# Kernel optimization log

Hardware: AMD Instinct MI355X
Metric: run time of the kernel (lower is better)

The kernel has to match this reference:

```python
import jax, jax.numpy as jnp
import numpy as np

GAMMA = 2.0
CONTEXT_WINDOW = 100


def setup_inputs() -> dict:
    key = jax.random.key(0)
    k1, k2 = jax.random.split(key)
    B, S, C = 64, 131072, 3
    inputs = jax.random.normal(k1, (B, S, C), dtype=jnp.float32)
    targets = jax.random.randint(k2, (B, S), 0, C, dtype=jnp.int32)
    alpha = jnp.array([0.25, 1.0, 1.0], dtype=jnp.float32)
    return {"inputs": inputs, "targets": targets, "alpha": alpha}


def _window_mask(targets, window):
    # mask[b, i] = True iff any positive target within +/- window of i;
    # rows with no positives are fully True (matches torch loop semantics).
    B, S = targets.shape
    pos = targets > 0                                   # (B, S) bool
    cs = jnp.cumsum(pos.astype(jnp.int32), axis=1)      # inclusive prefix sums
    c = jnp.concatenate([jnp.zeros((B, 1), jnp.int32), cs], axis=1)  # (B, S+1)
    idx = jnp.arange(S)
    hi = jnp.minimum(idx + window + 1, S)               # exclusive end
    lo = jnp.maximum(idx - window, 0)                   # inclusive start
    count = c[:, hi] - c[:, lo]                         # positives in window
    mask = count > 0
    has_pos = pos.any(axis=1, keepdims=True)
    return jnp.where(has_pos, mask, True)


def reference(inputs, targets, alpha):
    # inputs: (B, S, C) logits; targets: (B, S) class indices
    mask = _window_mask(targets, CONTEXT_WINDOW)                     # (B, S)
    logp = jax.nn.log_softmax(inputs, axis=-1)                       # (B, S, C)
    ce = -jnp.take_along_axis(logp, targets[..., None].astype(jnp.int32), axis=-1)[..., 0]
    p_t = jnp.exp(-ce)
    focal = alpha[targets] * (1.0 - p_t) ** GAMMA * ce               # (B, S)
    m = mask.astype(inputs.dtype)
    # masked mean == mean over selected elements in the torch version
    return jnp.sum(focal * m) / jnp.sum(m)
```

## Files before the change

kernel.cpp:

```cpp
#include <hip/hip_runtime.h>

#define BB 64
#define SS 131072
#define WIN 100
#define TILE 4096
#define NTHREADS 256
#define TILES_PER_ROW (SS / TILE)
#define NBLOCKS (BB * TILES_PER_ROW)
#define EXT (TILE + 2*WIN)
#define NWORDS ((EXT + 63) / 64)
#define SH_BYTES (NWORDS * 64)
#define K4TOT (SH_BYTES / 4)
#define SROUNDS ((K4TOT + NTHREADS - 1) / NTHREADS)
#define NGROUPS 4

typedef float  fx4 __attribute__((ext_vector_type(4)));
typedef int    ix4 __attribute__((ext_vector_type(4)));

__device__ __forceinline__ void process4(
    const fx4 c0, const fx4 c1, const fx4 c2,
    const int j0, const unsigned long long mw, const unsigned int tpack,
    const float a0, const float a1, const float a2,
    float& fsum_m, float& fsum_a, int& cnt_m)
{
    const float xs[12] = {c0.x, c0.y, c0.z, c0.w, c1.x, c1.y, c1.z, c1.w,
                          c2.x, c2.y, c2.z, c2.w};
    #pragma unroll
    for (int j = 0; j < 4; ++j) {
        const float x0 = xs[3*j], x1 = xs[3*j+1], x2 = xs[3*j+2];
        const int tv = (tpack >> (8 * j)) & 0xFF;
        const float mx = fmaxf(x0, fmaxf(x1, x2));
        const float mn = fminf(x0, fminf(x1, x2));
        const float md = fmaxf(fminf(x0, x1), fminf(fmaxf(x0, x1), x2));
        const float emd = __expf(md - mx);
        const float emn = __expf(mn - mx);
        const float sum = 1.0f + emd + emn;
        const float xt  = (tv == 0) ? x0 : ((tv == 1) ? x1 : x2);
        const float et  = (xt == mx) ? 1.0f : ((xt == md) ? emd : emn);
        const float ce  = __logf(sum) + (mx - xt);
        const float pt  = et * __frcp_rn(sum);
        const float w   = (tv == 0) ? a0 : ((tv == 1) ? a1 : a2);
        const float om  = 1.0f - pt;
        const float focal = w * om * om * ce;
        const bool  m   = (mw >> ((j0 & 63) + j)) & 1ULL;

        fsum_a += focal;
        fsum_m += m ? focal : 0.0f;
        cnt_m  += m ? 1 : 0;
    }
}

__global__ __launch_bounds__(NTHREADS, 5) void focal_main(
    const float* __restrict__ inputs, const int* __restrict__ targets,
    const float* __restrict__ alpha, double* __restrict__ slots)
{
    __shared__ __align__(16) unsigned char sh_t[SH_BYTES];
    __shared__ unsigned long long wbits[NWORDS];
    __shared__ unsigned long long mbits[NWORDS];
    __shared__ double red[(NTHREADS/64) * 4];

    const int t = threadIdx.x;
    const int b = blockIdx.x / TILES_PER_ROW;
    const int tile = blockIdx.x % TILES_PER_ROW;
    const int s0 = tile * TILE;
    const int ext_lo = (s0 - WIN > 0) ? (s0 - WIN) : 0;
    const int ext_hi = (s0 + TILE + WIN < SS) ? (s0 + TILE + WIN) : SS;
    const int ext_len = ext_hi - ext_lo;
    const int tr_lo = s0 - ext_lo;

    const float* inrow = inputs + (long)b * SS * 3;
    const fx4* gbase = (const fx4*)(inrow + (long)s0 * 3);
    const fx4* p0 = gbase + t * 3;
    const fx4* p1 = gbase + 768 + t * 3;
    const fx4* p2 = gbase + 1536 + t * 3;
    const fx4* p3 = gbase + 2304 + t * 3;
    const fx4 q0  = __builtin_nontemporal_load(p0 + 0);
    const fx4 q1  = __builtin_nontemporal_load(p0 + 1);
    const fx4 q2  = __builtin_nontemporal_load(p0 + 2);
    const fx4 q3  = __builtin_nontemporal_load(p1 + 0);
    const fx4 q4  = __builtin_nontemporal_load(p1 + 1);
    const fx4 q5  = __builtin_nontemporal_load(p1 + 2);
    const fx4 q6  = __builtin_nontemporal_load(p2 + 0);
    const fx4 q7  = __builtin_nontemporal_load(p2 + 1);
    const fx4 q8  = __builtin_nontemporal_load(p2 + 2);
    const fx4 q9  = __builtin_nontemporal_load(p3 + 0);
    const fx4 q10 = __builtin_nontemporal_load(p3 + 1);
    const fx4 q11 = __builtin_nontemporal_load(p3 + 2);

    const float a0 = alpha[0], a1 = alpha[1], a2 = alpha[2];

    const int* trow = targets + (long)b * SS;
    #pragma unroll
    for (int it = 0; it < SROUNDS; ++it) {
        const int k4 = it * NTHREADS + t;
        if (k4 < K4TOT) {
            unsigned int pk = 0;
            if (4 * k4 < ext_len) {
                const ix4 tv4 =
                    __builtin_nontemporal_load((const ix4*)(trow + ext_lo + 4 * k4));
                pk = (unsigned)(tv4.x & 3) | ((unsigned)(tv4.y & 3) << 8) |
                     ((unsigned)(tv4.z & 3) << 16) | ((unsigned)(tv4.w & 3) << 24);
            }
            ((unsigned int*)sh_t)[k4] = pk;
        }
    }
    __syncthreads();

    int cnt_p = 0;
    if (t < NWORDS) {
        const uint4* qp = (const uint4*)(sh_t + (t << 6));
        unsigned long long wv = 0;
        #pragma unroll
        for (int r = 0; r < 4; ++r) {
            const uint4 u = qp[r];
            unsigned int x, nz;
            x = u.x; nz = (x | (x >> 1)) & 0x01010101u;
            wv |= (unsigned long long)((nz * 0x01020408u) >> 24) << (r*16 + 0);
            x = u.y; nz = (x | (x >> 1)) & 0x01010101u;
            wv |= (unsigned long long)((nz * 0x01020408u) >> 24) << (r*16 + 4);
            x = u.z; nz = (x | (x >> 1)) & 0x01010101u;
            wv |= (unsigned long long)((nz * 0x01020408u) >> 24) << (r*16 + 8);
            x = u.w; nz = (x | (x >> 1)) & 0x01010101u;
            wv |= (unsigned long long)((nz * 0x01020408u) >> 24) << (r*16 + 12);
        }
        wbits[t] = wv;
        int lo_bit = tr_lo - (t << 6);        if (lo_bit < 0) lo_bit = 0;
        int hi_bit = tr_lo + TILE - (t << 6); if (hi_bit > 64) hi_bit = 64;
        if (hi_bit > lo_bit) {
            unsigned long long rm = (hi_bit >= 64) ? ~0ULL : ((1ULL << hi_bit) - 1);
            rm &= (~0ULL << lo_bit);
            cnt_p = __popcll(wv & rm);
        }
    }
    __syncthreads();

    if (t < NWORDS) {
        const unsigned long long a = (t >= 2) ? wbits[t-2] : 0ULL;
        const unsigned long long bw = (t >= 1) ? wbits[t-1] : 0ULL;
        const unsigned long long c = wbits[t];
        const unsigned long long d = (t+1 < NWORDS) ? wbits[t+1] : 0ULL;
        const unsigned long long e = (t+2 < NWORDS) ? wbits[t+2] : 0ULL;
        unsigned long long m = c ? ~0ULL : 0ULL;
        if (d) { const int lo = __builtin_ctzll(d) - 36;
                 m |= (lo <= 0) ? ~0ULL : (~0ULL << lo); }
        if (e) { const int lo = __builtin_ctzll(e) + 28;
                 if (lo <= 63) m |= (~0ULL << lo); }
        if (bw) { const int hi = 63 - __builtin_clzll(bw) + 36;
                  m |= (hi >= 63) ? ~0ULL : (~0ULL >> (63 - hi)); }
        if (a) { const int hi = 63 - __builtin_clzll(a) - 28;
                 if (hi >= 0) m |= (hi >= 63) ? ~0ULL : (~0ULL >> (63 - hi)); }
        mbits[t] = m;
    }
    __syncthreads();

    float fsum_m = 0.0f, fsum_a = 0.0f;
    int cnt_m = 0;
    {
        int j0 = tr_lo + t * 4;
        process4(q0, q1, q2, j0, mbits[j0 >> 6],
                 *(const unsigned int*)(sh_t + j0),
                 a0, a1, a2, fsum_m, fsum_a, cnt_m);
        j0 += 1024;
        process4(q3, q4, q5, j0, mbits[j0 >> 6],
                 *(const unsigned int*)(sh_t + j0),
                 a0, a1, a2, fsum_m, fsum_a, cnt_m);
        j0 += 1024;
        process4(q6, q7, q8, j0, mbits[j0 >> 6],
                 *(const unsigned int*)(sh_t + j0),
                 a0, a1, a2, fsum_m, fsum_a, cnt_m);
        j0 += 1024;
        process4(q9, q10, q11, j0, mbits[j0 >> 6],
                 *(const unsigned int*)(sh_t + j0),
                 a0, a1, a2, fsum_m, fsum_a, cnt_m);
    }

    const int wave = t >> 6, lane = t & 63;
    #pragma unroll
    for (int off = 32; off >= 1; off >>= 1) {
        fsum_m += __shfl_down(fsum_m, off);
        fsum_a += __shfl_down(fsum_a, off);
        cnt_m  += __shfl_down(cnt_m, off);
        cnt_p  += __shfl_down(cnt_p, off);
    }
    if (lane == 0) {
        red[wave*4]   = (double)fsum_m; red[wave*4+1] = (double)cnt_m;
        red[wave*4+2] = (double)fsum_a; red[wave*4+3] = (double)cnt_p;
    }
    __syncthreads();
    if (t == 0) {
        double sm = 0, sc = 0, sa = 0, sp = 0;
        #pragma unroll
        for (int w = 0; w < NTHREADS/64; ++w) {
            sm += red[w*4]; sc += red[w*4+1]; sa += red[w*4+2]; sp += red[w*4+3];
        }
        double* slot = slots + (long)blockIdx.x * 4;
        slot[0] = sm;
        slot[1] = sc;
        slot[2] = sa;
        slot[3] = sp;
    }
}

__global__ __launch_bounds__(1024) void focal_final(
    const double* __restrict__ slots, float* __restrict__ out)
{
    __shared__ double redA[16 * 2];
    __shared__ double crs[BB];
    __shared__ double crc[BB];
    const int t = threadIdx.x;
    const int wave = t >> 6, lane = t & 63;

    double sm = 0.0, sc = 0.0;
    for (int k = t; k < NBLOCKS; k += 1024) {
        sm += slots[(long)k * 4 + 0];
        sc += slots[(long)k * 4 + 1];
    }
    #pragma unroll
    for (int off = 32; off >= 1; off >>= 1) {
        sm += __shfl_down(sm, off);
        sc += __shfl_down(sc, off);
    }
    if (lane == 0) { redA[wave*2] = sm; redA[wave*2+1] = sc; }

    const int row = t >> 4;
    const int rpart = t & 15;
    const long base = (long)row * TILES_PER_ROW + rpart * 2;
    double rs = slots[base*4 + 2] + slots[(base+1)*4 + 2];
    double rp = slots[base*4 + 3] + slots[(base+1)*4 + 3];
    #pragma unroll
    for (int off = 8; off >= 1; off >>= 1) {
        rs += __shfl_down(rs, off, 16);
        rp += __shfl_down(rp, off, 16);
    }
    if (rpart == 0) { crs[row] = rs; crc[row] = rp; }
    __syncthreads();

    if (t == 0) {
        double a = 0.0, bsum = 0.0;
        #pragma unroll
        for (int w = 0; w < 16; ++w) { a += redA[w*2]; bsum += redA[w*2+1]; }
        double corr_s = 0.0, corr_c = 0.0;
        #pragma unroll
        for (int r = 0; r < BB; ++r) {
            if (crc[r] == 0.0) { corr_s += crs[r]; corr_c += (double)SS; }
        }
        out[0] = (float)((a + corr_s) / (bsum + corr_c));
    }
}

extern "C" void kernel_launch(void* const* d_in, const int* in_sizes, int n_in,
                              void* d_out, int out_size, void* d_ws, size_t ws_size,
                              hipStream_t stream) {
    const float* inputs  = (const float*)d_in[0];
    const int*   targets = (const int*)d_in[1];
    const float* alpha   = (const float*)d_in[2];
    float* out = (float*)d_out;

    double* slots = (double*)d_ws;

    focal_main<<<NBLOCKS, NTHREADS, 0, stream>>>(inputs, targets, alpha, slots);
    focal_final<<<1, 1024, 0, stream>>>(slots, out);
}
```

Measured before the change: 178.1 us.

## Coalesce logit loads per wave and transpose through double-buffered LDS

Each wave now owns a contiguous 1024-element slice and loads it as fully coalesced fx4 chunks: lane l reads consecutive vectors instead of strided triples. The chunks are staged in a per-wave double-buffered LDS area and re-read as each lane's three vectors. Only the next group's three vectors are prefetched, not all twelve up front, which lowers register pressure but reduces loads in flight. The extra LDS round trip and reduced early memory-level parallelism may offset the better coalescing.

Measured after the change: 172.0 us. -3.4%, faster.

```diff
diff --git a/kernel.cpp b/kernel.cpp
--- a/kernel.cpp
+++ b/kernel.cpp
@@ -5,6 +5,7 @@
 #define WIN 100
 #define TILE 4096
 #define NTHREADS 256
+#define NWAVES (NTHREADS / 64)
 #define TILES_PER_ROW (SS / TILE)
 #define NBLOCKS (BB * TILES_PER_ROW)
 #define EXT (TILE + 2*WIN)
@@ -12,7 +13,8 @@
 #define SH_BYTES (NWORDS * 64)
 #define K4TOT (SH_BYTES / 4)
 #define SROUNDS ((K4TOT + NTHREADS - 1) / NTHREADS)
-#define NGROUPS 4
+#define WGROUPS 4
+#define GF4 192
 
 typedef float  fx4 __attribute__((ext_vector_type(4)));
 typedef int    ix4 __attribute__((ext_vector_type(4)));
@@ -57,9 +59,11 @@
     __shared__ __align__(16) unsigned char sh_t[SH_BYTES];
     __shared__ unsigned long long wbits[NWORDS];
     __shared__ unsigned long long mbits[NWORDS];
-    __shared__ double red[(NTHREADS/64) * 4];
+    __shared__ fx4 lbuf[NWAVES][2][GF4];
+    __shared__ double red[NWAVES * 4];
 
     const int t = threadIdx.x;
+    const int w = t >> 6, l = t & 63;
     const int b = blockIdx.x / TILES_PER_ROW;
     const int tile = blockIdx.x % TILES_PER_ROW;
     const int s0 = tile * TILE;
@@ -69,25 +73,10 @@
     const int tr_lo = s0 - ext_lo;
 
     const float* inrow = inputs + (long)b * SS * 3;
-    const fx4* gbase = (const fx4*)(inrow + (long)s0 * 3);
-    const fx4* p0 = gbase + t * 3;
-    const fx4* p1 = gbase + 768 + t * 3;
-    const fx4* p2 = gbase + 1536 + t * 3;
-    const fx4* p3 = gbase + 2304 + t * 3;
-    const fx4 q0  = __builtin_nontemporal_load(p0 + 0);
-    const fx4 q1  = __builtin_nontemporal_load(p0 + 1);
-    const fx4 q2  = __builtin_nontemporal_load(p0 + 2);
-    const fx4 q3  = __builtin_nontemporal_load(p1 + 0);
-    const fx4 q4  = __builtin_nontemporal_load(p1 + 1);
-    const fx4 q5  = __builtin_nontemporal_load(p1 + 2);
-    const fx4 q6  = __builtin_nontemporal_load(p2 + 0);
-    const fx4 q7  = __builtin_nontemporal_load(p2 + 1);
-    const fx4 q8  = __builtin_nontemporal_load(p2 + 2);
-    const fx4 q9  = __builtin_nontemporal_load(p3 + 0);
-    const fx4 q10 = __builtin_nontemporal_load(p3 + 1);
-    const fx4 q11 = __builtin_nontemporal_load(p3 + 2);
-
-    const float a0 = alpha[0], a1 = alpha[1], a2 = alpha[2];
+    const fx4* gsrc = (const fx4*)(inrow + (long)(s0 + w * 1024) * 3);
+    fx4 q0 = __builtin_nontemporal_load(gsrc + l);
+    fx4 q1 = __builtin_nontemporal_load(gsrc + 64 + l);
+    fx4 q2 = __builtin_nontemporal_load(gsrc + 128 + l);
 
     const int* trow = targets + (long)b * SS;
     #pragma unroll
@@ -153,28 +142,30 @@
     }
     __syncthreads();
 
+    const float a0 = alpha[0], a1 = alpha[1], a2 = alpha[2];
     float fsum_m = 0.0f, fsum_a = 0.0f;
     int cnt_m = 0;
-    {
-        int j0 = tr_lo + t * 4;
-        process4(q0, q1, q2, j0, mbits[j0 >> 6],
+
+    #pragma unroll
+    for (int g = 0; g < WGROUPS; ++g) {
+        fx4* pb = lbuf[w][g & 1];
+        pb[l] = q0; pb[64 + l] = q1; pb[128 + l] = q2;
+        if (g + 1 < WGROUPS) {
+            const fx4* gn = gsrc + (g + 1) * GF4;
+            q0 = __builtin_nontemporal_load(gn + l);
+            q1 = __builtin_nontemporal_load(gn + 64 + l);
+            q2 = __builtin_nontemporal_load(gn + 128 + l);
+        }
+        const fx4 c0 = pb[3 * l];
+        const fx4 c1 = pb[3 * l + 1];
+        const fx4 c2 = pb[3 * l + 2];
+
+        const int j0 = tr_lo + w * 1024 + g * 256 + l * 4;
+        process4(c0, c1, c2, j0, mbits[j0 >> 6],
                  *(const unsigned int*)(sh_t + j0),
                  a0, a1, a2, fsum_m, fsum_a, cnt_m);
-        j0 += 1024;
-        process4(q3, q4, q5, j0, mbits[j0 >> 6],
-                 *(const unsigned int*)(sh_t + j0),
-                 a0, a1, a2, fsum_m, fsum_a, cnt_m);
-        j0 += 1024;
-        process4(q6, q7, q8, j0, mbits[j0 >> 6],
-                 *(const unsigned int*)(sh_t + j0),
-                 a0, a1, a2, fsum_m, fsum_a, cnt_m);
-        j0 += 1024;
-        process4(q9, q10, q11, j0, mbits[j0 >> 6],
-                 *(const unsigned int*)(sh_t + j0),
-                 a0, a1, a2, fsum_m, fsum_a, cnt_m);
-    }
-
-    const int wave = t >> 6, lane = t & 63;
+    }
+
     #pragma unroll
     for (int off = 32; off >= 1; off >>= 1) {
         fsum_m += __shfl_down(fsum_m, off);
@@ -182,16 +173,16 @@
         cnt_m  += __shfl_down(cnt_m, off);
         cnt_p  += __shfl_down(cnt_p, off);
     }
-    if (lane == 0) {
-        red[wave*4]   = (double)fsum_m; red[wave*4+1] = (double)cnt_m;
-        red[wave*4+2] = (double)fsum_a; red[wave*4+3] = (double)cnt_p;
+    if (l == 0) {
+        red[w*4]   = (double)fsum_m; red[w*4+1] = (double)cnt_m;
+        red[w*4+2] = (double)fsum_a; red[w*4+3] = (double)cnt_p;
     }
     __syncthreads();
     if (t == 0) {
         double sm = 0, sc = 0, sa = 0, sp = 0;
         #pragma unroll
-        for (int w = 0; w < NTHREADS/64; ++w) {
-            sm += red[w*4]; sc += red[w*4+1]; sa += red[w*4+2]; sp += red[w*4+3];
+        for (int v = 0; v < NWAVES; ++v) {
+            sm += red[v*4]; sc += red[v*4+1]; sa += red[v*4+2]; sp += red[v*4+3];
         }
         double* slot = slots + (long)blockIdx.x * 4;
         slot[0] = sm;
@@ -238,7 +229,7 @@
     if (t == 0) {
         double a = 0.0, bsum = 0.0;
         #pragma unroll
-        for (int w = 0; w < 16; ++w) { a += redA[w*2]; bsum += redA[w*2+1]; }
+        for (int v = 0; v < 16; ++v) { a += redA[v*2]; bsum += redA[v*2+1]; }
         double corr_s = 0.0, corr_c = 0.0;
         #pragma unroll
         for (int r = 0; r < BB; ++r) {
```
